# Optimization experiments

Measured on AMD Instinct MI355X. Metric: run time of the kernel, lower is better.

Reference implementation:

```python
import jax, jax.numpy as jnp
import numpy as np

N_UNITS = 1024
H = 16
D_K = N_UNITS // H
B = 4
T = 2048


def setup_inputs() -> dict:
    key = jax.random.key(0)
    ks = jax.random.split(key, 9)
    scale = 1.0 / np.sqrt(N_UNITS)
    return {
        "x": jax.random.normal(ks[0], (B * T, N_UNITS), dtype=jnp.float32),
        "Wq": jax.random.normal(ks[1], (N_UNITS, N_UNITS), dtype=jnp.float32) * scale,
        "bq": jax.random.normal(ks[2], (N_UNITS,), dtype=jnp.float32) * 0.01,
        "Wk": jax.random.normal(ks[3], (N_UNITS, N_UNITS), dtype=jnp.float32) * scale,
        "bk": jax.random.normal(ks[4], (N_UNITS,), dtype=jnp.float32) * 0.01,
        "Wv": jax.random.normal(ks[5], (N_UNITS, N_UNITS), dtype=jnp.float32) * scale,
        "bv": jax.random.normal(ks[6], (N_UNITS,), dtype=jnp.float32) * 0.01,
        "Wo": jax.random.normal(ks[7], (N_UNITS, N_UNITS), dtype=jnp.float32) * scale,
        "bo": jax.random.normal(ks[8], (N_UNITS,), dtype=jnp.float32) * 0.01,
        "batch_size": B,
    }


def reference(x, Wq, bq, Wk, bk, Wv, bv, Wo, bo, batch_size):
    # x: (batch*seq, n_units). Project then split into heads.
    q = (x @ Wq.T + bq).reshape(batch_size, -1, H, D_K)  # (b, t, h, d)
    k = (x @ Wk.T + bk).reshape(batch_size, -1, H, D_K)
    v = (x @ Wv.T + bv).reshape(batch_size, -1, H, D_K)
    scores = jnp.einsum("bqhd,bkhd->bhqk", q, k) / np.sqrt(D_K)
    att = jax.nn.softmax(scores, axis=-1)  # dropout=0.0 -> identity
    ctx = jnp.einsum("bhqk,bkhd->bqhd", att, v)
    ctx = ctx.reshape(-1, H * D_K)  # (batch*seq, n_units)
    return ctx @ Wo.T + bo
```

## Files before the change

kernel.cpp:

```cpp
#include <hip/hip_runtime.h>

typedef __bf16 bf16_t;
typedef __attribute__((ext_vector_type(8))) __bf16 bf16x8;
typedef __attribute__((ext_vector_type(4))) __bf16 bf16x4;
typedef __attribute__((ext_vector_type(4))) float f32x4;

#define M_TOT 8192
#define NU    1024
#define TSEQ  2048
#define NHEAD 16
#define DHEAD 64
#define BPAD  72
#define QSCALE 0.18033688011f

__device__ __forceinline__ void gload_lds16(const void* g, void* lds) {
    __builtin_amdgcn_global_load_lds(
        (const __attribute__((address_space(1))) void*)g,
        (__attribute__((address_space(3))) void*)lds,
        16, 0, 0);
}

__device__ __forceinline__ unsigned pk2(float a, float b) {
    const bf16_t x = (bf16_t)a, y = (bf16_t)b;
    return (unsigned)__builtin_bit_cast(unsigned short, x)
         | ((unsigned)__builtin_bit_cast(unsigned short, y) << 16);
}

__device__ __forceinline__ int fidx(int r, int k) {
    return ((((r >> 4) & 3) * 2 + (k >> 5)) << 9)
         + (((((k >> 3) & 3) << 4) + (r & 15)) << 3) + (k & 7);
}
__device__ __forceinline__ size_t fragK(int bh, int t, int d) {
    return (size_t)bh * (TSEQ * DHEAD) + (size_t)(t >> 6) * 4096 + fidx(t & 63, d);
}
__device__ __forceinline__ size_t fragV(int bh, int t, int d) {
    return (size_t)bh * (TSEQ * DHEAD) + (size_t)(t >> 6) * 4096 + fidx(d, t & 63);
}

__global__ __launch_bounds__(256)
void cvt_x(const float* __restrict__ x, bf16_t* __restrict__ xb)
{
    const int i = (blockIdx.x * 256 + threadIdx.x) * 8;
    const float4 a = *(const float4*)(x + i);
    const float4 b = *(const float4*)(x + i + 4);
    bf16x8 v;
    v[0] = (bf16_t)a.x; v[1] = (bf16_t)a.y; v[2] = (bf16_t)a.z; v[3] = (bf16_t)a.w;
    v[4] = (bf16_t)b.x; v[5] = (bf16_t)b.y; v[6] = (bf16_t)b.z; v[7] = (bf16_t)b.w;
    *(bf16x8*)(xb + i) = v;
}

__device__ __forceinline__ void cvt_frag_body(const float* __restrict__ src, bf16_t* __restrict__ dst)
{
    const int o8   = blockIdx.x * 256 + threadIdx.x;
    const int tile = o8 >> 9;
    const int c    = (o8 >> 6) & 7;
    const int s    = o8 & 63;
    const int r  = (tile >> 4) * 64 + ((c >> 1) * 16 + (s & 15));
    const int k  = (tile & 15) * 64 + ((c & 1) * 32 + ((s >> 4) * 8));
    const float4 a = *(const float4*)(src + (size_t)r * NU + k);
    const float4 b = *(const float4*)(src + (size_t)r * NU + k + 4);
    bf16x8 v;
    v[0] = (bf16_t)a.x; v[1] = (bf16_t)a.y; v[2] = (bf16_t)a.z; v[3] = (bf16_t)a.w;
    v[4] = (bf16_t)b.x; v[5] = (bf16_t)b.y; v[6] = (bf16_t)b.z; v[7] = (bf16_t)b.w;
    *(bf16x8*)(dst + (size_t)o8 * 8) = v;
}

__global__ __launch_bounds__(256)
void cvt_frag(const float* __restrict__ src, bf16_t* __restrict__ dst)
{
    cvt_frag_body(src, dst);
}

__global__ __launch_bounds__(256)
void cvt_frag_w(const float* __restrict__ Wq, const float* __restrict__ Wk,
                const float* __restrict__ Wv, const float* __restrict__ Wo,
                bf16_t* __restrict__ dst)
{
    const int z = blockIdx.z;
    const float* src = (z == 0) ? Wq : (z == 1 ? Wk : (z == 2 ? Wv : Wo));
    cvt_frag_body(src, dst + (size_t)z * NU * NU);
}

__global__ __launch_bounds__(256)
void gemm_qkv_f(const bf16_t* __restrict__ xf,
                const bf16_t* __restrict__ Wqf, const bf16_t* __restrict__ Wkf, const bf16_t* __restrict__ Wvf,
                const float* __restrict__ B0, const float* __restrict__ B1, const float* __restrict__ B2,
                bf16_t* __restrict__ O0, bf16_t* __restrict__ O1, bf16_t* __restrict__ O2)
{
    const int z = blockIdx.z;
    const bf16_t* Wf  = (z == 0) ? Wqf : (z == 1 ? Wkf : Wvf);
    const float* bias = (z == 0) ? B0 : (z == 1 ? B1 : B2);
    bf16_t* out       = (z == 0) ? O0 : (z == 1 ? O1 : O2);
    const float scale = (z == 0) ? QSCALE : 1.0f;

    __shared__ __attribute__((aligned(16))) bf16_t As[2 * 4096];
    __shared__ __attribute__((aligned(16))) bf16_t Bs[2 * 4096];

    const int tid = threadIdx.x;
    const int l   = tid & 63;
    const int w   = tid >> 6;
    const int wm  = w >> 1, wn = w & 1;
    const int l15 = l & 15, lq = l >> 4;
    const int bm  = blockIdx.y, bn = blockIdx.x;

    const bf16_t* gA[4];
    const bf16_t* gB[4];
#pragma unroll
    for (int i = 0; i < 4; ++i) {
        const int cc = w * 4 + i;
        gA[i] = xf + ((size_t)(bm * 2 + (cc >> 3)) * 16) * 4096 + (cc & 7) * 512 + l * 8;
        gB[i] = Wf + ((size_t)(bn * 2 + (cc >> 3)) * 16) * 4096 + (cc & 7) * 512 + l * 8;
    }

    f32x4 acc[4][4] = {};

    for (int kt = 0; kt < 16; ++kt) {
#pragma unroll
        for (int i = 0; i < 4; ++i) {
            const int cc = w * 4 + i;
            gload_lds16(gA[i] + (size_t)kt * 4096, &As[cc * 512]);
            gload_lds16(gB[i] + (size_t)kt * 4096, &Bs[cc * 512]);
        }
        __syncthreads();
#pragma unroll
        for (int ks = 0; ks < 2; ++ks) {
            bf16x8 af[4], bfr[4];
#pragma unroll
            for (int mt = 0; mt < 4; ++mt)
                af[mt] = *(const bf16x8*)&As[wm * 4096 + (mt * 2 + ks) * 512 + l * 8];
#pragma unroll
            for (int nt = 0; nt < 4; ++nt)
                bfr[nt] = *(const bf16x8*)&Bs[wn * 4096 + (nt * 2 + ks) * 512 + l * 8];
#pragma unroll
            for (int mt = 0; mt < 4; ++mt)
#pragma unroll
                for (int nt = 0; nt < 4; ++nt)
                    acc[mt][nt] = __builtin_amdgcn_mfma_f32_16x16x32_bf16(af[mt], bfr[nt], acc[mt][nt], 0, 0, 0);
        }
        __syncthreads();
    }

#pragma unroll
    for (int nt = 0; nt < 4; ++nt) {
        const int gn = bn * 128 + wn * 64 + nt * 16 + l15;
        const float bv = bias[gn];
#pragma unroll
        for (int mt = 0; mt < 4; ++mt) {
            const int rb = bm * 128 + wm * 64 + mt * 16 + lq * 4;
#pragma unroll
            for (int r = 0; r < 4; ++r) {
                const int gm = rb + r;
                const float v = (acc[mt][nt][r] + bv) * scale;
                const int b = gm >> 11, t = gm & (TSEQ - 1);
                const int h = gn >> 6,  d = gn & 63;
                const int bh = b * NHEAD + h;
                if (z == 0)
                    out[((size_t)bh * TSEQ + t) * DHEAD + d] = (bf16_t)v;
                else if (z == 1)
                    out[fragK(bh, t, d)] = (bf16_t)v;
                else
                    out[fragV(bh, t, d)] = (bf16_t)v;
            }
        }
    }
}

__global__ __launch_bounds__(256)
void gemm_out_f(const bf16_t* __restrict__ cf, const bf16_t* __restrict__ Wof,
                const float* __restrict__ bo, float* __restrict__ out)
{
    __shared__ __attribute__((aligned(16))) bf16_t As[2 * 4096];
    __shared__ __attribute__((aligned(16))) bf16_t Bs[2 * 4096];

    const int tid = threadIdx.x;
    const int l   = tid & 63;
    const int w   = tid >> 6;
    const int wm  = w >> 1, wn = w & 1;
    const int l15 = l & 15, lq = l >> 4;
    const int bm  = blockIdx.y, bn = blockIdx.x;
    const int b   = bm >> 4;

    const bf16_t* gB[4];
    size_t aoff[4];
#pragma unroll
    for (int i = 0; i < 4; ++i) {
        const int cc = w * 4 + i;
        aoff[i] = (((size_t)b * 16) * 32 + (bm & 15) * 2 + (cc >> 3)) * 4096 + (cc & 7) * 512 + l * 8;
        gB[i] = Wof + ((size_t)(bn * 2 + (cc >> 3)) * 16) * 4096 + (cc & 7) * 512 + l * 8;
    }

    f32x4 acc[4][4] = {};

    for (int kt = 0; kt < 16; ++kt) {
#pragma unroll
        for (int i = 0; i < 4; ++i) {
            const int cc = w * 4 + i;
            gload_lds16(cf + aoff[i] + (size_t)kt * (32 * 4096), &As[cc * 512]);
            gload_lds16(gB[i] + (size_t)kt * 4096, &Bs[cc * 512]);
        }
        __syncthreads();
#pragma unroll
        for (int ks = 0; ks < 2; ++ks) {
            bf16x8 af[4], bfr[4];
#pragma unroll
            for (int mt = 0; mt < 4; ++mt)
                af[mt] = *(const bf16x8*)&As[wm * 4096 + (mt * 2 + ks) * 512 + l * 8];
#pragma unroll
            for (int nt = 0; nt < 4; ++nt)
                bfr[nt] = *(const bf16x8*)&Bs[wn * 4096 + (nt * 2 + ks) * 512 + l * 8];
#pragma unroll
            for (int mt = 0; mt < 4; ++mt)
#pragma unroll
                for (int nt = 0; nt < 4; ++nt)
                    acc[mt][nt] = __builtin_amdgcn_mfma_f32_16x16x32_bf16(af[mt], bfr[nt], acc[mt][nt], 0, 0, 0);
        }
        __syncthreads();
    }

#pragma unroll
    for (int nt = 0; nt < 4; ++nt) {
        const int gn = bn * 128 + wn * 64 + nt * 16 + l15;
        const float bv = bo[gn];
#pragma unroll
        for (int mt = 0; mt < 4; ++mt) {
            const int rb = bm * 128 + wm * 64 + mt * 16 + lq * 4;
#pragma unroll
            for (int r = 0; r < 4; ++r)
                out[(size_t)(rb + r) * NU + gn] = acc[mt][nt][r] + bv;
        }
    }
}

__global__ __launch_bounds__(256)
void gemm_qkv(const bf16_t* __restrict__ A,
              const float* __restrict__ W0, const float* __restrict__ W1, const float* __restrict__ W2,
              const float* __restrict__ B0, const float* __restrict__ B1, const float* __restrict__ B2,
              bf16_t* __restrict__ O0, bf16_t* __restrict__ O1, bf16_t* __restrict__ O2)
{
    const int z = blockIdx.z;
    const float* W    = (z == 0) ? W0 : (z == 1 ? W1 : W2);
    const float* bias = (z == 0) ? B0 : (z == 1 ? B1 : B2);
    bf16_t* out       = (z == 0) ? O0 : (z == 1 ? O1 : O2);
    const float scale = (z == 0) ? QSCALE : 1.0f;

    __shared__ __attribute__((aligned(16))) bf16_t As[128 * 64];
    __shared__ __attribute__((aligned(16))) bf16_t Bs[128 * BPAD];

    const int tid = threadIdx.x;
    const int l = tid & 63, w = tid >> 6;
    const int wm = w >> 1, wn = w & 1;
    const int l15 = l & 15, lq = l >> 4;
    const int bm = blockIdx.y, bn = blockIdx.x;
    const int srow = l >> 3, scol = (l & 7) * 8;
    const bf16_t* gA = A + (size_t)(bm * 128 + srow) * NU + scol;
    const int sr = tid >> 4, sc = (tid & 15) * 4;
    const float* gW = W + (size_t)(bn * 128 + sr) * NU + sc;

    f32x4 acc[4][4] = {};
    float4 wreg[8];
#pragma unroll
    for (int i = 0; i < 8; ++i) wreg[i] = *(const float4*)(gW + (size_t)(i * 16) * NU);

    for (int k0 = 0; k0 < NU; k0 += 64) {
#pragma unroll
        for (int i = 0; i < 4; ++i) {
            const int r0 = i * 32 + w * 8;
            gload_lds16(gA + (size_t)r0 * NU + k0, &As[r0 * 64]);
        }
#pragma unroll
        for (int i = 0; i < 8; ++i) {
            bf16x4 wb;
            wb[0] = (bf16_t)wreg[i].x; wb[1] = (bf16_t)wreg[i].y;
            wb[2] = (bf16_t)wreg[i].z; wb[3] = (bf16_t)wreg[i].w;
            *(bf16x4*)&Bs[(i * 16 + sr) * BPAD + sc] = wb;
        }
        __syncthreads();
        if (k0 + 64 < NU) {
#pragma unroll
            for (int i = 0; i < 8; ++i)
                wreg[i] = *(const float4*)(gW + (size_t)(i * 16) * NU + k0 + 64);
        }
#pragma unroll
        for (int ks = 0; ks < 2; ++ks) {
            bf16x8 af[4], bfr[4];
#pragma unroll
            for (int mt = 0; mt < 4; ++mt)
                af[mt] = *(const bf16x8*)&As[(wm * 64 + mt * 16 + l15) * 64 + ks * 32 + lq * 8];
#pragma unroll
            for (int nt = 0; nt < 4; ++nt)
                bfr[nt] = *(const bf16x8*)&Bs[(wn * 64 + nt * 16 + l15) * BPAD + ks * 32 + lq * 8];
#pragma unroll
            for (int mt = 0; mt < 4; ++mt)
#pragma unroll
                for (int nt = 0; nt < 4; ++nt)
                    acc[mt][nt] = __builtin_amdgcn_mfma_f32_16x16x32_bf16(af[mt], bfr[nt], acc[mt][nt], 0, 0, 0);
        }
        __syncthreads();
    }

#pragma unroll
    for (int nt = 0; nt < 4; ++nt) {
        const int gn = bn * 128 + wn * 64 + nt * 16 + l15;
        const float bv = bias[gn];
#pragma unroll
        for (int mt = 0; mt < 4; ++mt) {
            const int rb = bm * 128 + wm * 64 + mt * 16 + lq * 4;
#pragma unroll
            for (int r = 0; r < 4; ++r) {
                const int gm = rb + r;
                const float v = (acc[mt][nt][r] + bv) * scale;
                const int b = gm >> 11, t = gm & (TSEQ - 1);
                const int h = gn >> 6,  d = gn & 63;
                const int bh = b * NHEAD + h;
                if (z == 0)      out[((size_t)bh * TSEQ + t) * DHEAD + d] = (bf16_t)v;
                else if (z == 1) out[fragK(bh, t, d)] = (bf16_t)v;
                else             out[fragV(bh, t, d)] = (bf16_t)v;
            }
        }
    }
}

__global__ __launch_bounds__(256)
void gemm_out(const bf16_t* __restrict__ ctx, const float* __restrict__ Wo,
              const float* __restrict__ bo, float* __restrict__ out)
{
    __shared__ __attribute__((aligned(16))) bf16_t As[128 * 64];
    __shared__ __attribute__((aligned(16))) bf16_t Bs[128 * BPAD];

    const int tid = threadIdx.x;
    const int l = tid & 63, w = tid >> 6;
    const int wm = w >> 1, wn = w & 1;
    const int l15 = l & 15, lq = l >> 4;
    const int bm = blockIdx.y, bn = blockIdx.x;
    const int srow = l >> 3, scol = (l & 7) * 8;
    const int b = bm >> 4;
    const bf16_t* gA = ctx + (size_t)b * (NHEAD * TSEQ * DHEAD)
                           + (size_t)((bm & 15) * 128 + srow) * DHEAD + scol;
    const int sr = tid >> 4, sc = (tid & 15) * 4;
    const float* gW = Wo + (size_t)(bn * 128 + sr) * NU + sc;

    f32x4 acc[4][4] = {};
    float4 wreg[8];
#pragma unroll
    for (int i = 0; i < 8; ++i) wreg[i] = *(const float4*)(gW + (size_t)(i * 16) * NU);

    for (int k0 = 0; k0 < NU; k0 += 64) {
#pragma unroll
        for (int i = 0; i < 4; ++i) {
            const int r0 = i * 32 + w * 8;
            gload_lds16(gA + (size_t)r0 * DHEAD + ((size_t)k0 << 11), &As[r0 * 64]);
        }
#pragma unroll
        for (int i = 0; i < 8; ++i) {
            bf16x4 wb;
            wb[0] = (bf16_t)wreg[i].x; wb[1] = (bf16_t)wreg[i].y;
            wb[2] = (bf16_t)wreg[i].z; wb[3] = (bf16_t)wreg[i].w;
            *(bf16x4*)&Bs[(i * 16 + sr) * BPAD + sc] = wb;
        }
        __syncthreads();
        if (k0 + 64 < NU) {
#pragma unroll
            for (int i = 0; i < 8; ++i)
                wreg[i] = *(const float4*)(gW + (size_t)(i * 16) * NU + k0 + 64);
        }
#pragma unroll
        for (int ks = 0; ks < 2; ++ks) {
            bf16x8 af[4], bfr[4];
#pragma unroll
            for (int mt = 0; mt < 4; ++mt)
                af[mt] = *(const bf16x8*)&As[(wm * 64 + mt * 16 + l15) * 64 + ks * 32 + lq * 8];
#pragma unroll
            for (int nt = 0; nt < 4; ++nt)
                bfr[nt] = *(const bf16x8*)&Bs[(wn * 64 + nt * 16 + l15) * BPAD + ks * 32 + lq * 8];
#pragma unroll
            for (int mt = 0; mt < 4; ++mt)
#pragma unroll
                for (int nt = 0; nt < 4; ++nt)
                    acc[mt][nt] = __builtin_amdgcn_mfma_f32_16x16x32_bf16(af[mt], bfr[nt], acc[mt][nt], 0, 0, 0);
        }
        __syncthreads();
    }

#pragma unroll
    for (int nt = 0; nt < 4; ++nt) {
        const int gn = bn * 128 + wn * 64 + nt * 16 + l15;
        const float bv = bo[gn];
#pragma unroll
        for (int mt = 0; mt < 4; ++mt) {
            const int rb = bm * 128 + wm * 64 + mt * 16 + lq * 4;
#pragma unroll
            for (int r = 0; r < 4; ++r)
                out[(size_t)(rb + r) * NU + gn] = acc[mt][nt][r] + bv;
        }
    }
}

template <bool FRAGOUT>
__global__ __launch_bounds__(256, 3)
void attn_fwd(const bf16_t* __restrict__ Q, const bf16_t* __restrict__ Kf,
              const bf16_t* __restrict__ Vf, bf16_t* __restrict__ Cw)
{
    __shared__ __attribute__((aligned(16))) bf16_t Ps[4][4 * 512];

    const int tid = threadIdx.x;
    const int l   = tid & 63;
    const int w   = tid >> 6;
    const int l15 = l & 15, lq = l >> 4;

    const int id = blockIdx.x;
    const int bh = (id & 7) * 8 + ((id >> 3) & 7);
    const int qt = id >> 6;
    const int q0 = qt * 128 + w * 32;

    const bf16_t* Qb = Q  + (size_t)bh * TSEQ * DHEAD;
    const bf16_t* Kb = Kf + (size_t)bh * TSEQ * DHEAD + l * 8;
    const bf16_t* Vb = Vf + (size_t)bh * TSEQ * DHEAD + l * 8;

    bf16x8 qf[2][2];
#pragma unroll
    for (int mt = 0; mt < 2; ++mt)
#pragma unroll
        for (int ks = 0; ks < 2; ++ks)
            qf[mt][ks] = *(const bf16x8*)(Qb + (size_t)(q0 + mt * 16 + l15) * DHEAD + ks * 32 + lq * 8);

    bf16x8 ones;
#pragma unroll
    for (int j = 0; j < 8; ++j) ones[j] = (bf16_t)1.0f;

    f32x4 cacc[2][4] = {};
    f32x4 lacc[2] = {};

    int* PsI = (int*)&Ps[w][0];

    for (int kt = 0; kt < TSEQ / 64; ++kt) {
        const bf16_t* kb = Kb + kt * 4096;
        const bf16_t* vb = Vb + kt * 4096;

        bf16x8 kf[8];
#pragma unroll
        for (int c = 0; c < 8; ++c) kf[c] = *(const bf16x8*)(kb + c * 512);

        f32x4 st[4][2] = {};
#pragma unroll
        for (int ks = 0; ks < 2; ++ks)
#pragma unroll
            for (int nt = 0; nt < 4; ++nt)
#pragma unroll
                for (int mt = 0; mt < 2; ++mt)
                    st[nt][mt] = __builtin_amdgcn_mfma_f32_16x16x32_bf16(kf[nt * 2 + ks], qf[mt][ks], st[nt][mt], 0, 0, 0);

#pragma unroll
        for (int nt = 0; nt < 4; ++nt)
#pragma unroll
            for (int mt = 0; mt < 2; ++mt) {
                const float p0 = __builtin_amdgcn_exp2f(st[nt][mt][0]);
                const float p1 = __builtin_amdgcn_exp2f(st[nt][mt][1]);
                const float p2 = __builtin_amdgcn_exp2f(st[nt][mt][2]);
                const float p3 = __builtin_amdgcn_exp2f(st[nt][mt][3]);
                const int base = (mt * 2 + (nt >> 1)) * 256
                               + ((nt & 1) * 2 + (lq >> 1)) * 64 + l15 * 4;
                PsI[base + ((lq * 2 + 0) & 3)] = (int)pk2(p0, p1);
                PsI[base + ((lq * 2 + 1) & 3)] = (int)pk2(p2, p3);
            }

        bf16x8 vf[8];
#pragma unroll
        for (int c = 0; c < 8; ++c) vf[c] = *(const bf16x8*)(vb + c * 512);

#pragma unroll
        for (int kv = 0; kv < 2; ++kv) {
            bf16x8 pf[2];
#pragma unroll
            for (int mt = 0; mt < 2; ++mt)
                pf[mt] = *(const bf16x8*)&Ps[w][(mt * 2 + kv) * 512 + l * 8];
#pragma unroll
            for (int mt = 0; mt < 2; ++mt) {
                lacc[mt] = __builtin_amdgcn_mfma_f32_16x16x32_bf16(ones, pf[mt], lacc[mt], 0, 0, 0);
#pragma unroll
                for (int dt = 0; dt < 4; ++dt)
                    cacc[mt][dt] = __builtin_amdgcn_mfma_f32_16x16x32_bf16(vf[dt * 2 + kv], pf[mt], cacc[mt][dt], 0, 0, 0);
            }
        }
    }

#pragma unroll
    for (int mt = 0; mt < 2; ++mt) {
        const float inv = 1.0f / lacc[mt][0];
        const int q = q0 + mt * 16 + l15;
#pragma unroll
        for (int dt = 0; dt < 4; ++dt) {
            bf16x4 cv;
#pragma unroll
            for (int r = 0; r < 4; ++r) cv[r] = (bf16_t)(cacc[mt][dt][r] * inv);
            if (FRAGOUT) {
                const int qr = q & 63;
                const size_t base = ((size_t)bh * 32 + (q >> 6)) * 4096;
                const int d0 = dt * 16 + lq * 4;
                const int addr = ((((qr >> 4) & 3) * 2 + (d0 >> 5)) << 9)
                               + (((((d0 >> 3) & 3) << 4) + (qr & 15)) << 3) + (d0 & 7);
                *(bf16x4*)&Cw[base + addr] = cv;
            } else {
                *(bf16x4*)&Cw[((size_t)bh * TSEQ + q) * DHEAD + dt * 16 + lq * 4] = cv;
            }
        }
    }
}

__global__ void diag_fill(float* out, int n, float val)
{
    int i = blockIdx.x * blockDim.x + threadIdx.x;
    if (i < n) out[i] = val;
}

extern "C" void kernel_launch(void* const* d_in, const int* in_sizes, int n_in,
                              void* d_out, int out_size, void* d_ws, size_t ws_size,
                              hipStream_t stream)
{
    const float* x  = (const float*)d_in[0];
    const float* Wq = (const float*)d_in[1];
    const float* bq = (const float*)d_in[2];
    const float* Wk = (const float*)d_in[3];
    const float* bk = (const float*)d_in[4];
    const float* Wv = (const float*)d_in[5];
    const float* bv = (const float*)d_in[6];
    const float* Wo = (const float*)d_in[7];
    const float* bo = (const float*)d_in[8];

    const size_t SLOT = (size_t)M_TOT * NU;
    const size_t WSZ  = (size_t)NU * NU;
    const size_t need_fast = (2 * SLOT + 4 * WSZ) * sizeof(bf16_t);
    const size_t need_min  = 2 * SLOT * sizeof(bf16_t);

    bf16_t* Qw = (bf16_t*)d_out;
    bf16_t* Kw = Qw + SLOT;

    if (ws_size >= need_fast) {
        bf16_t* Xf  = (bf16_t*)d_ws;
        bf16_t* Vt  = Xf + SLOT;
        bf16_t* Wf4 = Vt + SLOT;
        bf16_t* Cf  = Xf;

        cvt_frag<<<dim3(M_TOT * NU / (256 * 8)), 256, 0, stream>>>(x, Xf);
        cvt_frag_w<<<dim3(NU * NU / (256 * 8), 1, 4), 256, 0, stream>>>(Wq, Wk, Wv, Wo, Wf4);
        gemm_qkv_f<<<dim3(NU / 128, M_TOT / 128, 3), 256, 0, stream>>>(
            Xf, Wf4, Wf4 + WSZ, Wf4 + 2 * WSZ, bq, bk, bv, Qw, Kw, Vt);
        attn_fwd<true><<<dim3(1024), 256, 0, stream>>>(Qw, Kw, Vt, Cf);
        gemm_out_f<<<dim3(NU / 128, M_TOT / 128), 256, 0, stream>>>(Cf, Wf4 + 3 * WSZ, bo, (float*)d_out);
    } else if (ws_size >= need_min) {
        bf16_t* Xb = (bf16_t*)d_ws;
        bf16_t* Vt = Xb + SLOT;
        bf16_t* Cw = Xb;
        cvt_x<<<dim3(M_TOT * NU / (256 * 8)), 256, 0, stream>>>(x, Xb);
        gemm_qkv<<<dim3(NU / 128, M_TOT / 128, 3), 256, 0, stream>>>(
            Xb, Wq, Wk, Wv, bq, bk, bv, Qw, Kw, Vt);
        attn_fwd<false><<<dim3(1024), 256, 0, stream>>>(Qw, Kw, Vt, Cw);
        gemm_out<<<dim3(NU / 128, M_TOT / 128), 256, 0, stream>>>(Cw, Wo, bo, (float*)d_out);
    } else {
        diag_fill<<<(out_size + 255) / 256, 256, 0, stream>>>((float*)d_out, out_size, 9.0f);
    }
}
```

Measured before the change: 295.9 us.

## Stage K/V tiles through double-buffered LDS with async global-to-LDS loads

After: 296.9 us. Within noise of the previous version (+0.4%).

```diff
diff --git a/kernel.cpp b/kernel.cpp
--- a/kernel.cpp
+++ b/kernel.cpp
@@ -4,6 +4,7 @@
 typedef __attribute__((ext_vector_type(8))) __bf16 bf16x8;
 typedef __attribute__((ext_vector_type(4))) __bf16 bf16x4;
 typedef __attribute__((ext_vector_type(4))) float f32x4;
+typedef __attribute__((ext_vector_type(2))) int i32x2;
 
 #define M_TOT 8192
 #define NU    1024
@@ -401,6 +402,8 @@
               const bf16_t* __restrict__ Vf, bf16_t* __restrict__ Cw)
 {
     __shared__ __attribute__((aligned(16))) bf16_t Ps[4][4 * 512];
+    __shared__ __attribute__((aligned(16))) bf16_t Kd[2][4096];
+    __shared__ __attribute__((aligned(16))) bf16_t Vd[2][4096];
 
     const int tid = threadIdx.x;
     const int l   = tid & 63;
@@ -432,13 +435,35 @@
 
     int* PsI = (int*)&Ps[w][0];
 
-    for (int kt = 0; kt < TSEQ / 64; ++kt) {
-        const bf16_t* kb = Kb + kt * 4096;
-        const bf16_t* vb = Vb + kt * 4096;
+    const int co = (w & 1) * 4;
+    const bf16_t* sbase = (w < 2) ? Kb : Vb;
+
+#define STAGE(buf, ktn)                                                          \
+    do {                                                                         \
+        const bf16_t* s_ = sbase + (size_t)(ktn) * 4096 + co * 512;              \
+        bf16_t* d_ = ((w < 2) ? &Kd[(buf)][0] : &Vd[(buf)][0]) + co * 512;       \
+        _Pragma("unroll")                                                        \
+        for (int c_ = 0; c_ < 4; ++c_)                                           \
+            gload_lds16(s_ + c_ * 512, d_ + c_ * 512);                           \
+    } while (0)
+
+    __builtin_amdgcn_sched_barrier(0);
+    STAGE(0, 0);
+    __builtin_amdgcn_sched_barrier(0);
+
+    const int NT = TSEQ / 64;
+    for (int kt = 0; kt < NT; ++kt) {
+        const int cur = kt & 1;
+        if (kt + 1 < NT) {
+            STAGE(cur ^ 1, kt + 1);
+            asm volatile("s_waitcnt vmcnt(4)\n\ts_barrier" ::: "memory");
+        } else {
+            asm volatile("s_waitcnt vmcnt(0)\n\ts_barrier" ::: "memory");
+        }
 
         bf16x8 kf[8];
 #pragma unroll
-        for (int c = 0; c < 8; ++c) kf[c] = *(const bf16x8*)(kb + c * 512);
+        for (int c = 0; c < 8; ++c) kf[c] = *(const bf16x8*)&Kd[cur][c * 512 + l * 8];
 
         f32x4 st[4][2] = {};
 #pragma unroll
@@ -458,14 +483,16 @@
                 const float p2 = __builtin_amdgcn_exp2f(st[nt][mt][2]);
                 const float p3 = __builtin_amdgcn_exp2f(st[nt][mt][3]);
                 const int base = (mt * 2 + (nt >> 1)) * 256
-                               + ((nt & 1) * 2 + (lq >> 1)) * 64 + l15 * 4;
-                PsI[base + ((lq * 2 + 0) & 3)] = (int)pk2(p0, p1);
-                PsI[base + ((lq * 2 + 1) & 3)] = (int)pk2(p2, p3);
+                               + ((nt & 1) * 2 + (lq >> 1)) * 64 + l15 * 4 + (lq & 1) * 2;
+                i32x2 pw;
+                pw[0] = (int)pk2(p0, p1);
+                pw[1] = (int)pk2(p2, p3);
+                *(i32x2*)&PsI[base] = pw;
             }
 
         bf16x8 vf[8];
 #pragma unroll
-        for (int c = 0; c < 8; ++c) vf[c] = *(const bf16x8*)(vb + c * 512);
+        for (int c = 0; c < 8; ++c) vf[c] = *(const bf16x8*)&Vd[cur][c * 512 + l * 8];
 
 #pragma unroll
         for (int kv = 0; kv < 2; ++kv) {
@@ -481,7 +508,10 @@
                     cacc[mt][dt] = __builtin_amdgcn_mfma_f32_16x16x32_bf16(vf[dt * 2 + kv], pf[mt], cacc[mt][dt], 0, 0, 0);
             }
         }
-    }
+
+        asm volatile("s_barrier" ::: "memory");
+    }
+#undef STAGE
 
 #pragma unroll
     for (int mt = 0; mt < 2; ++mt) {
```
